# Kernel tuning notes

Measured on AMD Instinct MI355X. Metric: run time of the kernel, lower is better.

## Reference

```python
import jax, jax.numpy as jnp
import numpy as np

NUM, NUM_TOP, COBJ = 32, 32, 4   # num = MBS*ncobj, num_top, cobj_size = k//2
B, D, H = 300, 256, 256          # bag_size, feature dim, relation hidden
K_OBJ = 8                        # k (output cobj size)
FEA0 = 2 * NUM * COBJ            # orig_fea leading dim = MBS*K with K=2*ncobj*cobj_size


def setup_inputs() -> dict:
    key = jax.random.key(0)
    ks = jax.random.split(key, 8)
    return {
        "orig_fea": jax.random.normal(ks[0], (FEA0, B, D), dtype=jnp.float32),
        "ind0": jax.random.randint(ks[1], (NUM, NUM_TOP, COBJ), 0, B, dtype=jnp.int32),
        "ind1": jax.random.randint(ks[2], (NUM, NUM_TOP, COBJ), 0, B, dtype=jnp.int32),
        "k": K_OBJ,
        "W1a": jax.random.normal(ks[3], (D, H), dtype=jnp.float32) * (1.0 / np.sqrt(D)),
        "W1b": jax.random.normal(ks[4], (D, H), dtype=jnp.float32) * (1.0 / np.sqrt(D)),
        "b1": jnp.zeros((H,), dtype=jnp.float32),
        "W2": jax.random.normal(ks[5], (H, 1), dtype=jnp.float32) * (1.0 / np.sqrt(H)),
        "b2": jnp.zeros((1,), dtype=jnp.float32),
    }


def reference(orig_fea, ind0, ind1, k, W1a, W1b, b1, W2, b2):
    num, num_top, cobj = ind0.shape
    bag = orig_fea.shape[1]
    d = orig_fea.shape[2]
    # create_ids: stride bag_size over cobj positions -> [num, L], L = num_top*cobj
    off = (bag * jnp.arange(cobj, dtype=ind0.dtype))
    ids0 = (ind0 + off).reshape(num, -1)
    ids1 = (ind1 + off).reshape(num, -1)
    # rsolo_fea = reshape(orig_fea, [num, 2, pool, D]); pool = cobj*bag
    pool = (orig_fea.shape[0] * bag) // (2 * num)
    rsolo = orig_fea.reshape(num, 2, pool, d)
    # gather per-side features (dedup+inverse-gather in the original is an
    # optimization; direct gather yields the identical score matrix)
    f0 = jnp.take_along_axis(rsolo[:, 0], ids0[..., None], axis=1)  # [num, L, D]
    f1 = jnp.take_along_axis(rsolo[:, 1], ids1[..., None], axis=1)  # [num, L, D]
    # relation unit: score(a,b) = MLP(concat(f0_a, f1_b)) -> [num, L, L, 1]
    h0 = jnp.einsum('nad,dh->nah', f0, W1a)          # [num, L, H]
    h1 = jnp.einsum('nbd,dh->nbh', f1, W1b)          # [num, L, H]
    h = jax.nn.relu(h0[:, :, None, :] + h1[:, None, :, :] + b1)  # [num, L, L, H]
    scores = jnp.einsum('nabh,ho->nabo', h, W2) + b2              # [num, L, L, 1]
    # sum_kxk_patches with patch size k//2
    kp = k // 2
    L = num_top * cobj
    hk = L // kp
    scores = scores.reshape(num, hk, kp, hk, kp, 1).sum(axis=(2, 4))  # [num, m, l, 1]
    m = l = num_top
    scores = scores.reshape(num, m * l, 1)
    # get_pairs
    pairs = jnp.stack(jnp.meshgrid(jnp.arange(m, dtype=jnp.int32),
                                   jnp.arange(l, dtype=jnp.int32), indexing='ij'),
                      axis=-1).reshape(1, m * l, 2)
    pairs = jnp.broadcast_to(pairs, (num, m * l, 2))
    return scores, pairs
```

## Files before the change

kernel.cpp:

```cpp
#include <hip/hip_runtime.h>

#define NUMB 32
#define NTOP 32
#define COBJ 4
#define BAG  300
#define DD   256
#define HHID 256
#define LL   128
#define POOL 1200

__global__ __launch_bounds__(256) void k_h01(
    const float* __restrict__ fea,
    const int*   __restrict__ ind0,
    const int*   __restrict__ ind1,
    const float* __restrict__ W1a,
    const float* __restrict__ W1b,
    const float* __restrict__ b1,
    float*       __restrict__ Hout)
{
    const int bm = blockIdx.x >> 2;
    const int bn = blockIdx.x & 3;
    const int t  = threadIdx.x;

    __shared__ float As[16][68];
    __shared__ float Bs[16][68];

    const int side = (bm >= 64);

    const int lr = t >> 2;
    const int kc = (t & 3) << 2;
    const int grow = bm * 64 + lr;
    const int n_   = (grow >> 7) & 31;
    const int a_   = grow & 127;
    const int id   = (side ? ind1 : ind0)[n_ * LL + a_] + BAG * (a_ & 3);
    const float* arow = fea + (size_t)((n_ * 2 + side) * POOL + id) * DD;
    const float* Wm   = side ? W1b : W1a;

    const int tn = t & 15, tm = t >> 4;

    float c[4][4] = {{0.f,0.f,0.f,0.f},{0.f,0.f,0.f,0.f},
                     {0.f,0.f,0.f,0.f},{0.f,0.f,0.f,0.f}};

    for (int kk = 0; kk < DD; kk += 16) {
        float4 av = *(const float4*)(arow + kk + kc);
        float4 bv = *(const float4*)(Wm + (size_t)(kk + tm) * HHID + bn * 64 + tn * 4);
        __syncthreads();
        As[kc + 0][lr] = av.x;
        As[kc + 1][lr] = av.y;
        As[kc + 2][lr] = av.z;
        As[kc + 3][lr] = av.w;
        *(float4*)&Bs[tm][tn * 4] = bv;
        __syncthreads();
#pragma unroll
        for (int k = 0; k < 16; ++k) {
            float4 af = *(float4*)&As[k][tm * 4];
            float4 bf = *(float4*)&Bs[k][tn * 4];
            float ar[4] = {af.x, af.y, af.z, af.w};
            float br[4] = {bf.x, bf.y, bf.z, bf.w};
#pragma unroll
            for (int r = 0; r < 4; ++r)
#pragma unroll
                for (int s = 0; s < 4; ++s)
                    c[r][s] = fmaf(ar[r], br[s], c[r][s]);
        }
    }

    const int colb = bn * 64 + tn * 4;
    float4 bias;
    if (!side) bias = *(const float4*)(b1 + colb);
    else { bias.x = bias.y = bias.z = bias.w = 0.f; }
#pragma unroll
    for (int r = 0; r < 4; ++r) {
        const int row = bm * 64 + tm * 4 + r;
        float4 o;
        o.x = c[r][0] + bias.x;
        o.y = c[r][1] + bias.y;
        o.z = c[r][2] + bias.z;
        o.w = c[r][3] + bias.w;
        *(float4*)(Hout + (size_t)row * HHID + colb) = o;
    }
}

__global__ __launch_bounds__(256) void k_init(
    const float* __restrict__ b2, float* __restrict__ out)
{
    const int NS = NUMB * NTOP * NTOP;
    int i = blockIdx.x * 256 + threadIdx.x;
    if (i < NS) {
        out[i] = 16.0f * b2[0];
    } else if (i < 3 * NS) {
        int j = i - NS;
        int p = (j >> 1) & 1023;
        out[i] = (j & 1) ? (float)(p & 31) : (float)(p >> 5);
    }
}

__global__ __launch_bounds__(256) void k_pair(
    const float* __restrict__ Hbuf,
    const float* __restrict__ W2,
    float*       __restrict__ out)
{
    int b = blockIdx.x;
    const int hs = b & 3;  b >>= 2;
    const int jt = b & 1;  b >>= 1;
    const int it = b & 1;  b >>= 1;
    const int n  = b;

    __shared__ float s0[64 * 64];
    __shared__ float s1[64 * 64];
    __shared__ float w2s[64];

    const int t = threadIdx.x;
    const float* H0 = Hbuf + ((size_t)(n * LL) + it * 64) * HHID + hs * 64;
    const float* H1 = Hbuf + ((size_t)(NUMB * LL) + n * LL + jt * 64) * HHID + hs * 64;

#pragma unroll
    for (int rep = 0; rep < 4; ++rep) {
        int idx = rep * 256 + t;
        int row = idx >> 4;
        int f   = idx & 15;
        int fs  = f ^ ((row >> 2) & 7);
        float4 v0 = *(const float4*)(H0 + (size_t)row * HHID + f * 4);
        float4 v1 = *(const float4*)(H1 + (size_t)row * HHID + f * 4);
        *(float4*)&s0[row * 64 + fs * 4] = v0;
        *(float4*)&s1[row * 64 + fs * 4] = v1;
    }
    if (t < 16) *(float4*)&w2s[t * 4] = *(const float4*)(W2 + hs * 64 + t * 4);
    __syncthreads();

    const int jl = t & 15, il = t >> 4;
    float acc[4][4] = {{0.f,0.f,0.f,0.f},{0.f,0.f,0.f,0.f},
                       {0.f,0.f,0.f,0.f},{0.f,0.f,0.f,0.f}};

#pragma unroll
    for (int f = 0; f < 16; ++f) {
        float4 w = *(float4*)&w2s[f * 4];
        float4 a[4], bb[4];
#pragma unroll
        for (int r = 0; r < 4; ++r)
            a[r] = *(float4*)&s0[(il * 4 + r) * 64 + (f ^ (il & 7)) * 4];
#pragma unroll
        for (int s = 0; s < 4; ++s)
            bb[s] = *(float4*)&s1[(jl * 4 + s) * 64 + (f ^ (jl & 7)) * 4];
#pragma unroll
        for (int r = 0; r < 4; ++r)
#pragma unroll
            for (int s = 0; s < 4; ++s) {
                acc[r][s] = fmaf(fmaxf(a[r].x + bb[s].x, 0.f), w.x, acc[r][s]);
                acc[r][s] = fmaf(fmaxf(a[r].y + bb[s].y, 0.f), w.y, acc[r][s]);
                acc[r][s] = fmaf(fmaxf(a[r].z + bb[s].z, 0.f), w.z, acc[r][s]);
                acc[r][s] = fmaf(fmaxf(a[r].w + bb[s].w, 0.f), w.w, acc[r][s]);
            }
    }

    float sum = 0.f;
#pragma unroll
    for (int r = 0; r < 4; ++r)
#pragma unroll
        for (int s = 0; s < 4; ++s) sum += acc[r][s];

    atomicAdd(out + n * 1024 + (it * 16 + il) * 32 + jt * 16 + jl, sum);
}

extern "C" void kernel_launch(void* const* d_in, const int* in_sizes, int n_in,
                              void* d_out, int out_size, void* d_ws, size_t ws_size,
                              hipStream_t stream)
{
    const float* fea  = (const float*)d_in[0];
    const int*   ind0 = (const int*)  d_in[1];
    const int*   ind1 = (const int*)  d_in[2];
    const float* W1a  = (const float*)d_in[4];
    const float* W1b  = (const float*)d_in[5];
    const float* b1   = (const float*)d_in[6];
    const float* W2   = (const float*)d_in[7];
    const float* b2   = (const float*)d_in[8];
    float* out  = (float*)d_out;
    float* Hbuf = (float*)d_ws;

    hipLaunchKernelGGL(k_h01, dim3(512), dim3(256), 0, stream,
                       fea, ind0, ind1, W1a, W1b, b1, Hbuf);
    hipLaunchKernelGGL(k_init, dim3(384), dim3(256), 0, stream, b2, out);
    hipLaunchKernelGGL(k_pair, dim3(512), dim3(256), 0, stream,
                       Hbuf, W2, out);
}
```

Before: 142.6 us.

## Use bf16 MFMA for hidden GEMM and packed fp16 dot for pair stage

The weights are pre-transposed and converted to bf16 in a prep kernel, which also absorbs the output init. The gathered-feature GEMM now uses MFMA 16x16x32 bf16 with global_load_lds staging, and writes the hidden activations as fp16. The pair kernel loads fp16 tiles directly into LDS and computes relu(a+b)·W2 with packed half adds and fdot2. This is meant to cut FP32 ALU work and memory traffic in both stages, at the cost of reduced precision in the hidden activations and the relu sums.

```diff
diff --git a/kernel.cpp b/kernel.cpp
--- a/kernel.cpp
+++ b/kernel.cpp
@@ -1,131 +1,193 @@
 #include <hip/hip_runtime.h>
 
 #define NUMB 32
-#define NTOP 32
-#define COBJ 4
+#define LL   128
+#define POOL 1200
 #define BAG  300
 #define DD   256
-#define HHID 256
-#define LL   128
-#define POOL 1200
-
-__global__ __launch_bounds__(256) void k_h01(
+#define HH   256
+#define NS   (NUMB*32*32)
+
+using bf16x8 = __bf16    __attribute__((ext_vector_type(8)));
+using f32x4  = float     __attribute__((ext_vector_type(4)));
+using fp16x2 = __fp16    __attribute__((ext_vector_type(2)));
+using h16x2  = _Float16  __attribute__((ext_vector_type(2)));
+using h16x8  = _Float16  __attribute__((ext_vector_type(8)));
+
+typedef const __attribute__((address_space(1))) unsigned int* gas_t;
+typedef       __attribute__((address_space(3))) unsigned int* las_t;
+
+static __device__ __forceinline__ unsigned short f2bf(float x) {
+    unsigned u = __float_as_uint(x);
+    return (unsigned short)((u + 0x7FFFu + ((u >> 16) & 1u)) >> 16);
+}
+
+static __device__ __forceinline__ float pkh(float a, float b) {
+    fp16x2 p = __builtin_amdgcn_cvt_pkrtz(a, b);
+    return __builtin_bit_cast(float, p);
+}
+
+__global__ __launch_bounds__(256) void k_prep(
+    const float* __restrict__ W1a, const float* __restrict__ W1b,
+    const float* __restrict__ b2,
+    unsigned short* __restrict__ WtP, float* __restrict__ out)
+{
+    const int blk = blockIdx.x, t = threadIdx.x;
+    if (blk < 32) {
+        const int side = blk >> 4, kc = blk & 15;
+        const float* W = side ? W1b : W1a;
+        __shared__ float T[16][257];
+        const int row = t >> 4, c = t & 15;
+#pragma unroll
+        for (int i = 0; i < 4; ++i) {
+            int col4 = c + i * 16;
+            float4 v = *(const float4*)(W + (size_t)(kc * 16 + row) * HH + col4 * 4);
+            T[row][col4 * 4 + 0] = v.x; T[row][col4 * 4 + 1] = v.y;
+            T[row][col4 * 4 + 2] = v.z; T[row][col4 * 4 + 3] = v.w;
+        }
+        __syncthreads();
+        const int n = t, ht = n >> 6, nn = n & 63;
+#pragma unroll
+        for (int j = 0; j < 2; ++j) {
+            unsigned short tmp[8] __attribute__((aligned(16)));
+#pragma unroll
+            for (int e = 0; e < 8; ++e) tmp[e] = f2bf(T[j * 8 + e][n]);
+            int U = kc * 2 + j;
+            int pos = U ^ (nn & 7);
+            size_t unit = ((size_t)((side * 4 + ht) * 64 + nn)) * 32 + pos;
+            *(float4*)(WtP + unit * 8) = *(float4*)tmp;
+        }
+    } else {
+        int i = (blk - 32) * 256 + t;
+        if (i < NS) {
+            out[i] = 16.0f * b2[0];
+        } else if (i < 3 * NS) {
+            int j = i - NS;
+            int p = (j >> 1) & 1023;
+            out[i] = (j & 1) ? (float)(p & 31) : (float)(p >> 5);
+        }
+    }
+}
+
+__global__ __launch_bounds__(256) void k_gemm(
     const float* __restrict__ fea,
     const int*   __restrict__ ind0,
     const int*   __restrict__ ind1,
-    const float* __restrict__ W1a,
-    const float* __restrict__ W1b,
     const float* __restrict__ b1,
-    float*       __restrict__ Hout)
-{
-    const int bm = blockIdx.x >> 2;
-    const int bn = blockIdx.x & 3;
-    const int t  = threadIdx.x;
-
-    __shared__ float As[16][68];
-    __shared__ float Bs[16][68];
-
-    const int side = (bm >= 64);
-
-    const int lr = t >> 2;
-    const int kc = (t & 3) << 2;
-    const int grow = bm * 64 + lr;
-    const int n_   = (grow >> 7) & 31;
-    const int a_   = grow & 127;
-    const int id   = (side ? ind1 : ind0)[n_ * LL + a_] + BAG * (a_ & 3);
-    const float* arow = fea + (size_t)((n_ * 2 + side) * POOL + id) * DD;
-    const float* Wm   = side ? W1b : W1a;
-
-    const int tn = t & 15, tm = t >> 4;
-
-    float c[4][4] = {{0.f,0.f,0.f,0.f},{0.f,0.f,0.f,0.f},
-                     {0.f,0.f,0.f,0.f},{0.f,0.f,0.f,0.f}};
-
-    for (int kk = 0; kk < DD; kk += 16) {
-        float4 av = *(const float4*)(arow + kk + kc);
-        float4 bv = *(const float4*)(Wm + (size_t)(kk + tm) * HHID + bn * 64 + tn * 4);
-        __syncthreads();
-        As[kc + 0][lr] = av.x;
-        As[kc + 1][lr] = av.y;
-        As[kc + 2][lr] = av.z;
-        As[kc + 3][lr] = av.w;
-        *(float4*)&Bs[tm][tn * 4] = bv;
-        __syncthreads();
-#pragma unroll
-        for (int k = 0; k < 16; ++k) {
-            float4 af = *(float4*)&As[k][tm * 4];
-            float4 bf = *(float4*)&Bs[k][tn * 4];
-            float ar[4] = {af.x, af.y, af.z, af.w};
-            float br[4] = {bf.x, bf.y, bf.z, bf.w};
-#pragma unroll
-            for (int r = 0; r < 4; ++r)
-#pragma unroll
-                for (int s = 0; s < 4; ++s)
-                    c[r][s] = fmaf(ar[r], br[s], c[r][s]);
-        }
-    }
-
-    const int colb = bn * 64 + tn * 4;
-    float4 bias;
-    if (!side) bias = *(const float4*)(b1 + colb);
-    else { bias.x = bias.y = bias.z = bias.w = 0.f; }
-#pragma unroll
-    for (int r = 0; r < 4; ++r) {
-        const int row = bm * 64 + tm * 4 + r;
-        float4 o;
-        o.x = c[r][0] + bias.x;
-        o.y = c[r][1] + bias.y;
-        o.z = c[r][2] + bias.z;
-        o.w = c[r][3] + bias.w;
-        *(float4*)(Hout + (size_t)row * HHID + colb) = o;
-    }
-}
-
-__global__ __launch_bounds__(256) void k_init(
-    const float* __restrict__ b2, float* __restrict__ out)
-{
-    const int NS = NUMB * NTOP * NTOP;
-    int i = blockIdx.x * 256 + threadIdx.x;
-    if (i < NS) {
-        out[i] = 16.0f * b2[0];
-    } else if (i < 3 * NS) {
-        int j = i - NS;
-        int p = (j >> 1) & 1023;
-        out[i] = (j & 1) ? (float)(p & 31) : (float)(p >> 5);
+    const unsigned short* __restrict__ WtP,
+    unsigned short* __restrict__ Hh)
+{
+    __shared__ unsigned short As[64 * 256] __attribute__((aligned(16)));
+    __shared__ unsigned short Bs[64 * 256] __attribute__((aligned(16)));
+
+    int b = blockIdx.x;
+    const int ht = b & 3, rt = b >> 2;
+    const int side = rt >> 6;
+    const int R0 = rt * 64;
+    const int t = threadIdx.x, w = t >> 6, lane = t & 63;
+
+    const unsigned short* Wbase = WtP + ((size_t)(side * 4 + ht)) * 64 * 256;
+#pragma unroll
+    for (int i = 0; i < 8; ++i) {
+        int chunk = w * 8 + i;
+        __builtin_amdgcn_global_load_lds(
+            (gas_t)(const void*)(Wbase + chunk * 512 + lane * 8),
+            (las_t)(void*)(As + chunk * 512),
+            16, 0, 0);
+    }
+
+    {
+        const int lr = t >> 2;
+        const int g = R0 + lr;
+        const int rs = g & 4095, n_ = rs >> 7, a_ = rs & 127;
+        const int id = (side ? ind1 : ind0)[n_ * LL + a_] + BAG * (a_ & 3);
+        const float* arow = fea + (size_t)((n_ * 2 + side) * POOL + id) * DD;
+        const int sw = lr & 7;
+#pragma unroll
+        for (int j0 = 0; j0 < 16; ++j0) {
+            int jj = j0 * 4 + (t & 3);
+            float4 v = *(const float4*)(arow + jj * 4);
+            unsigned short tmp[4] __attribute__((aligned(8)));
+            tmp[0] = f2bf(v.x); tmp[1] = f2bf(v.y);
+            tmp[2] = f2bf(v.z); tmp[3] = f2bf(v.w);
+            int u = jj >> 1, pos = u ^ sw;
+            *(double*)&Bs[lr * 256 + pos * 8 + (jj & 1) * 4] = *(double*)tmp;
+        }
+    }
+    __syncthreads();
+
+    const int l15 = lane & 15, q = lane >> 4;
+    f32x4 acc[4] = {};
+#pragma unroll
+    for (int kk = 0; kk < 8; ++kk) {
+        const int u = kk * 4 + q;
+        const int hr = w * 16 + l15;
+        bf16x8 af = *(const bf16x8*)&As[hr * 256 + (u ^ (hr & 7)) * 8];
+        bf16x8 bf[4];
+#pragma unroll
+        for (int rb = 0; rb < 4; ++rb) {
+            int r = rb * 16 + l15;
+            bf[rb] = *(const bf16x8*)&Bs[r * 256 + (u ^ (r & 7)) * 8];
+        }
+#pragma unroll
+        for (int rb = 0; rb < 4; ++rb)
+            acc[rb] = __builtin_amdgcn_mfma_f32_16x16x32_bf16(af, bf[rb], acc[rb], 0, 0, 0);
+    }
+
+    const int hbase = ht * 64 + w * 16 + q * 4;
+    float4 bias = make_float4(0.f, 0.f, 0.f, 0.f);
+    if (side == 0) bias = *(const float4*)(b1 + hbase);
+#pragma unroll
+    for (int rb = 0; rb < 4; ++rb) {
+        int frow = R0 + rb * 16 + l15;
+        float2 pk;
+        pk.x = pkh(acc[rb][0] + bias.x, acc[rb][1] + bias.y);
+        pk.y = pkh(acc[rb][2] + bias.z, acc[rb][3] + bias.w);
+        *(float2*)&Hh[(size_t)frow * HH + hbase] = pk;
     }
 }
 
 __global__ __launch_bounds__(256) void k_pair(
-    const float* __restrict__ Hbuf,
+    const unsigned short* __restrict__ Hh,
     const float* __restrict__ W2,
     float*       __restrict__ out)
 {
+    __shared__ unsigned short s0[64 * 64] __attribute__((aligned(16)));
+    __shared__ unsigned short s1[64 * 64] __attribute__((aligned(16)));
+    __shared__ unsigned short w2s[64]     __attribute__((aligned(16)));
+
     int b = blockIdx.x;
     const int hs = b & 3;  b >>= 2;
     const int jt = b & 1;  b >>= 1;
     const int it = b & 1;  b >>= 1;
     const int n  = b;
-
-    __shared__ float s0[64 * 64];
-    __shared__ float s1[64 * 64];
-    __shared__ float w2s[64];
-
-    const int t = threadIdx.x;
-    const float* H0 = Hbuf + ((size_t)(n * LL) + it * 64) * HHID + hs * 64;
-    const float* H1 = Hbuf + ((size_t)(NUMB * LL) + n * LL + jt * 64) * HHID + hs * 64;
-
-#pragma unroll
-    for (int rep = 0; rep < 4; ++rep) {
-        int idx = rep * 256 + t;
-        int row = idx >> 4;
-        int f   = idx & 15;
-        int fs  = f ^ ((row >> 2) & 7);
-        float4 v0 = *(const float4*)(H0 + (size_t)row * HHID + f * 4);
-        float4 v1 = *(const float4*)(H1 + (size_t)row * HHID + f * 4);
-        *(float4*)&s0[row * 64 + fs * 4] = v0;
-        *(float4*)&s1[row * 64 + fs * 4] = v1;
-    }
-    if (t < 16) *(float4*)&w2s[t * 4] = *(const float4*)(W2 + hs * 64 + t * 4);
+    const int t = threadIdx.x, w = t >> 6, lane = t & 63;
+
+    const size_t base0 = ((size_t)(n * LL) + it * 64) * HH + hs * 64;
+    const size_t base1 = ((size_t)(NUMB * LL + n * LL) + jt * 64) * HH + hs * 64;
+
+    {
+        const int lrow = lane >> 3, posslot = lane & 7;
+#pragma unroll
+        for (int i = 0; i < 2; ++i) {
+            int chunk = w * 2 + i;
+            int row = chunk * 8 + lrow;
+            int f = posslot ^ ((row >> 2) & 7);
+            __builtin_amdgcn_global_load_lds(
+                (gas_t)(const void*)(Hh + base0 + (size_t)row * HH + f * 8),
+                (las_t)(void*)(s0 + chunk * 512), 16, 0, 0);
+            __builtin_amdgcn_global_load_lds(
+                (gas_t)(const void*)(Hh + base1 + (size_t)row * HH + f * 8),
+                (las_t)(void*)(s1 + chunk * 512), 16, 0, 0);
+        }
+    }
+    if (t < 16) {
+        float4 v = *(const float4*)(W2 + hs * 64 + t * 4);
+        float2 pk;
+        pk.x = pkh(v.x, v.y);
+        pk.y = pkh(v.z, v.w);
+        *(float2*)&w2s[t * 4] = pk;
+    }
     __syncthreads();
 
     const int jl = t & 15, il = t >> 4;
@@ -133,33 +195,37 @@
                        {0.f,0.f,0.f,0.f},{0.f,0.f,0.f,0.f}};
 
 #pragma unroll
-    for (int f = 0; f < 16; ++f) {
-        float4 w = *(float4*)&w2s[f * 4];
-        float4 a[4], bb[4];
+    for (int f = 0; f < 8; ++f) {
+        h16x8 wv = *(const h16x8*)&w2s[f * 8];
+        const h16x2* wp = (const h16x2*)&wv;
+        h16x8 av[4], bv[4];
 #pragma unroll
         for (int r = 0; r < 4; ++r)
-            a[r] = *(float4*)&s0[(il * 4 + r) * 64 + (f ^ (il & 7)) * 4];
+            av[r] = *(const h16x8*)&s0[(il * 4 + r) * 64 + (f ^ (il & 7)) * 8];
 #pragma unroll
         for (int s = 0; s < 4; ++s)
-            bb[s] = *(float4*)&s1[(jl * 4 + s) * 64 + (f ^ (jl & 7)) * 4];
+            bv[s] = *(const h16x8*)&s1[(jl * 4 + s) * 64 + (f ^ (jl & 7)) * 8];
+        const h16x8 zero = {0, 0, 0, 0, 0, 0, 0, 0};
 #pragma unroll
         for (int r = 0; r < 4; ++r)
 #pragma unroll
             for (int s = 0; s < 4; ++s) {
-                acc[r][s] = fmaf(fmaxf(a[r].x + bb[s].x, 0.f), w.x, acc[r][s]);
-                acc[r][s] = fmaf(fmaxf(a[r].y + bb[s].y, 0.f), w.y, acc[r][s]);
-                acc[r][s] = fmaf(fmaxf(a[r].z + bb[s].z, 0.f), w.z, acc[r][s]);
-                acc[r][s] = fmaf(fmaxf(a[r].w + bb[s].w, 0.f), w.w, acc[r][s]);
+                h16x8 sum = av[r] + bv[s];
+                sum = __builtin_elementwise_max(sum, zero);
+                const h16x2* sp = (const h16x2*)&sum;
+#pragma unroll
+                for (int u = 0; u < 4; ++u)
+                    acc[r][s] = __builtin_amdgcn_fdot2(sp[u], wp[u], acc[r][s], false);
             }
     }
 
-    float sum = 0.f;
+    float total = 0.f;
 #pragma unroll
     for (int r = 0; r < 4; ++r)
 #pragma unroll
-        for (int s = 0; s < 4; ++s) sum += acc[r][s];
-
-    atomicAdd(out + n * 1024 + (it * 16 + il) * 32 + jt * 16 + jl, sum);
+        for (int s = 0; s < 4; ++s) total += acc[r][s];
+
+    atomicAdd(out + n * 1024 + (it * 16 + il) * 32 + jt * 16 + jl, total);
 }
 
 extern "C" void kernel_launch(void* const* d_in, const int* in_sizes, int n_in,
@@ -174,12 +240,15 @@
     const float* b1   = (const float*)d_in[6];
     const float* W2   = (const float*)d_in[7];
     const float* b2   = (const float*)d_in[8];
-    float* out  = (float*)d_out;
-    float* Hbuf = (float*)d_ws;
-
-    hipLaunchKernelGGL(k_h01, dim3(512), dim3(256), 0, stream,
-                       fea, ind0, ind1, W1a, W1b, b1, Hbuf);
-    hipLaunchKernelGGL(k_init, dim3(384), dim3(256), 0, stream, b2, out);
+    float* out = (float*)d_out;
+
+    unsigned short* WtP = (unsigned short*)d_ws;
+    unsigned short* Hh  = (unsigned short*)((char*)d_ws + 512 * 1024);
+
+    hipLaunchKernelGGL(k_prep, dim3(416), dim3(256), 0, stream,
+                       W1a, W1b, b2, WtP, out);
+    hipLaunchKernelGGL(k_gemm, dim3(512), dim3(256), 0, stream,
+                       fea, ind0, ind1, b1, WtP, Hh);
     hipLaunchKernelGGL(k_pair, dim3(512), dim3(256), 0, stream,
-                       Hbuf, W2, out);
-}
+                       Hh, W2, out);
+}
```

Result: faster. 131.2 us (-8.0%).
